# Kernel tuning notes

Measured on AMD Instinct MI355X. Metric: run time of the kernel, lower is better.

Reference implementation:

```python
import jax, jax.numpy as jnp
import numpy as np

C = 1024        # BIGNET_DIM
GS = 128        # group_size
R = 4           # lora_dim
NL = 12         # 4 blocks x 3 QLoRALinear
N = 4096        # batch
NG = C * C // GS  # 8192 groups per layer
EPS = 1e-5


def dequant4(q4, norm):
    # q4: [NG, GS//2] int32 in [0,255] (two nibbles per byte), norm: [NG,1] f32
    low = q4 & 0xF
    high = (q4 >> 4) & 0xF
    # interleave: even positions = low nibble, odd = high nibble
    q8 = jnp.stack([low, high], axis=-1).reshape(q4.shape[0], GS)
    w = (q8.astype(jnp.float32) / 15.0 * 2.0 - 1.0) * norm
    return w.reshape(C, C)  # [out_features, in_features]


def qlora_linear(x, q4, norm, a, b):
    # base 4-bit dequant matmul + low-rank LoRA add (bias=False)
    w = dequant4(q4, norm)
    return x @ w.T + (x @ a.T) @ b.T  # [N,C]


def block(x, q4s, norms, As, Bs):
    h = qlora_linear(x, q4s[0], norms[0], As[0], Bs[0])
    h = jax.nn.relu(h)
    h = qlora_linear(h, q4s[1], norms[1], As[1], Bs[1])
    h = jax.nn.relu(h)
    h = qlora_linear(h, q4s[2], norms[2], As[2], Bs[2])
    return h + x  # residual


def layer_norm(x, g, b):
    mu = jnp.mean(x, axis=-1, keepdims=True)
    var = jnp.var(x, axis=-1, keepdims=True)
    return (x - mu) * jax.lax.rsqrt(var + EPS) * g + b


def setup_inputs() -> dict:
    key = jax.random.key(0)
    ks = jax.random.split(key, 5)
    x = jax.random.normal(ks[0], (N, C), dtype=jnp.float32)
    w_q4 = jax.random.randint(ks[1], (NL, NG, GS // 2), 0, 256, dtype=jnp.int32)
    w_norm = jax.random.uniform(ks[2], (NL, NG, 1), dtype=jnp.float32, minval=0.01, maxval=0.1)
    lora_a = jax.random.normal(ks[3], (NL, R, C), dtype=jnp.float32) * 0.02
    lora_b = jax.random.normal(ks[4], (NL, C, R), dtype=jnp.float32) * 0.02
    ln_g = jnp.ones((2, C), dtype=jnp.float32)
    ln_b = jnp.zeros((2, C), dtype=jnp.float32)
    return {"x": x, "w_q4": w_q4, "w_norm": w_norm, "lora_a": lora_a,
            "lora_b": lora_b, "ln_g": ln_g, "ln_b": ln_b}


def reference(x, w_q4, w_norm, lora_a, lora_b, ln_g, ln_b):
    h = block(x, w_q4[0:3], w_norm[0:3], lora_a[0:3], lora_b[0:3])
    h = layer_norm(h, ln_g[0], ln_b[0])
    h = block(h, w_q4[3:6], w_norm[3:6], lora_a[3:6], lora_b[3:6])
    h = block(h, w_q4[6:9], w_norm[6:9], lora_a[6:9], lora_b[6:9])
    h = layer_norm(h, ln_g[1], ln_b[1])
    h = block(h, w_q4[9:12], w_norm[9:12], lora_a[9:12], lora_b[9:12])
    return h
```

## Files before the change

### kernel.cpp

```cpp
#include <hip/hip_runtime.h>

#define CD 1024
#define NB 4096

typedef __attribute__((ext_vector_type(8))) short short8;
typedef __attribute__((ext_vector_type(4))) short short4v;
typedef __attribute__((ext_vector_type(4))) float f32x4;
typedef __attribute__((ext_vector_type(4))) int int4v;

typedef __attribute__((address_space(1))) const void gv_t;
typedef __attribute__((address_space(3))) void lv_t;
#define GLOAD16(g, l) __builtin_amdgcn_global_load_lds((gv_t*)(g), (lv_t*)(l), 16, 0, 0)

__device__ __forceinline__ short f2bf(float f) {
  unsigned u = __float_as_uint(f);
  u = (u + 0x7FFFu + ((u >> 16) & 1u)) >> 16;
  return (short)u;
}
__device__ __forceinline__ float bf2f(short s) {
  return __uint_as_float(((unsigned)(unsigned short)s) << 16);
}

__global__ __launch_bounds__(256) void cvtx_kernel(const float* __restrict__ x,
                                                   short* __restrict__ xb) {
  int i = (blockIdx.x * 256 + threadIdx.x) * 8;
  f32x4 a = *(const f32x4*)(x + i);
  f32x4 b = *(const f32x4*)(x + i + 4);
  short8 o;
  o[0] = f2bf(a[0]); o[1] = f2bf(a[1]); o[2] = f2bf(a[2]); o[3] = f2bf(a[3]);
  o[4] = f2bf(b[0]); o[5] = f2bf(b[1]); o[6] = f2bf(b[2]); o[7] = f2bf(b[3]);
  *(short8*)(xb + i) = o;
}

__global__ __launch_bounds__(256) void deq_kernel(const int* __restrict__ q4,
                                                  const float* __restrict__ nrm,
                                                  const float* __restrict__ la,
                                                  const float* __restrict__ lb,
                                                  short* __restrict__ Wb) {
  int tidg = blockIdx.x * 256 + threadIdx.x;
  int w0 = tidg * 4;
  int l = w0 >> 19;
  int wl = w0 & 524287;
  int g = wl >> 6;
  int j0 = wl & 63;
  int o = g >> 3;
  int kb = ((g & 7) << 7) + (j0 << 1);
  int4v q = *(const int4v*)(q4 + w0);
  float n = nrm[(l << 13) + g];
  float s = n * (2.0f / 15.0f);
  f32x4 B = *(const f32x4*)(lb + (((l << 10) + o) << 2));
  const float* A = la + (l << 12);
  float Ar[4][8];
#pragma unroll
  for (int r = 0; r < 4; ++r) {
    f32x4 u = *(const f32x4*)(A + r * CD + kb);
    f32x4 v = *(const f32x4*)(A + r * CD + kb + 4);
    Ar[r][0] = u[0]; Ar[r][1] = u[1]; Ar[r][2] = u[2]; Ar[r][3] = u[3];
    Ar[r][4] = v[0]; Ar[r][5] = v[1]; Ar[r][6] = v[2]; Ar[r][7] = v[3];
  }
  short8 outv;
#pragma unroll
  for (int p = 0; p < 8; ++p) {
    int qw = q[p >> 1];
    int nib = (qw >> ((p & 1) << 2)) & 15;
    float wv = (float)nib * s - n;
    wv += B[0] * Ar[0][p] + B[1] * Ar[1][p] + B[2] * Ar[2][p] + B[3] * Ar[3][p];
    outv[p] = f2bf(wv);
  }
  *(short8*)(Wb + (l << 20) + (o << 10) + kb) = outv;
}

template <int EPI>
__global__ __launch_bounds__(256) void qgemm(const short* __restrict__ Act,
                                             const short* __restrict__ W,
                                             const short* __restrict__ Res,
                                             void* __restrict__ Out) {
  __shared__ __align__(16) short lds[2][2][128 * 64];
  const int tid = threadIdx.x;
  const int lane = tid & 63;
  const int wid = tid >> 6;
  const int wr = wid >> 1, wc = wid & 1;
  const int m0 = blockIdx.x * 128;
  const int o0 = blockIdx.y * 128;

  const int srow = (wid << 5) + (lane >> 3);
  const int gch = (lane & 7) ^ (lane >> 3);
  const short* aptr[4];
  const short* bptr[4];
#pragma unroll
  for (int i = 0; i < 4; ++i) {
    int r = srow + i * 8;
    aptr[i] = Act + (long)(m0 + r) * CD + (gch << 3);
    bptr[i] = W + (long)(o0 + r) * CD + (gch << 3);
  }

  auto stage = [&](int t, int buf) {
    const int koff = t << 6;
#pragma unroll
    for (int i = 0; i < 4; ++i) {
      GLOAD16(aptr[i] + koff, &lds[buf][0][((wid << 5) + (i << 3)) << 6]);
      GLOAD16(bptr[i] + koff, &lds[buf][1][((wid << 5) + (i << 3)) << 6]);
    }
  };

  f32x4 acc[4][4] = {};
  const int frow = lane & 15;
  const int fch = lane >> 4;
  const int fsw = lane & 7;

  stage(0, 0);
  for (int t = 0; t < 16; ++t) {
    __syncthreads();
    if (t < 15) stage(t + 1, (t + 1) & 1);
    const short* La = lds[t & 1][0];
    const short* Lb = lds[t & 1][1];
#pragma unroll
    for (int kk = 0; kk < 2; ++kk) {
      short8 af[4], bfr[4];
#pragma unroll
      for (int m = 0; m < 4; ++m) {
        int row = (wr << 6) + (m << 4) + frow;
        int ch = ((kk << 2) + fch) ^ fsw;
        af[m] = *(const short8*)(La + (row << 6) + (ch << 3));
      }
#pragma unroll
      for (int nn = 0; nn < 4; ++nn) {
        int row = (wc << 6) + (nn << 4) + frow;
        int ch = ((kk << 2) + fch) ^ fsw;
        bfr[nn] = *(const short8*)(Lb + (row << 6) + (ch << 3));
      }
#pragma unroll
      for (int m = 0; m < 4; ++m)
#pragma unroll
        for (int nn = 0; nn < 4; ++nn)
          acc[m][nn] = __builtin_amdgcn_mfma_f32_16x16x32_bf16(af[m], bfr[nn], acc[m][nn], 0, 0, 0);
    }
  }

  const int colb = o0 + (wc << 6) + frow;
  const int rowb = m0 + (wr << 6) + (fch << 2);
#pragma unroll
  for (int m = 0; m < 4; ++m) {
#pragma unroll
    for (int nn = 0; nn < 4; ++nn) {
#pragma unroll
      for (int r = 0; r < 4; ++r) {
        int row = rowb + (m << 4) + r;
        int col = colb + (nn << 4);
        float v = acc[m][nn][r];
        if (EPI == 0) {
          v = fmaxf(v, 0.0f);
          ((short*)Out)[(long)row * CD + col] = f2bf(v);
        } else if (EPI == 2) {
          v += bf2f(Res[(long)row * CD + col]);
          ((short*)Out)[(long)row * CD + col] = f2bf(v);
        } else {
          v += bf2f(Res[(long)row * CD + col]);
          ((float*)Out)[(long)row * CD + col] = v;
        }
      }
    }
  }
}

__global__ __launch_bounds__(256) void ln_kernel(const short* __restrict__ in,
                                                 short* __restrict__ out,
                                                 const float* __restrict__ g,
                                                 const float* __restrict__ b) {
  __shared__ float rs_[4], rq_[4];
  int row = blockIdx.x, tid = threadIdx.x;
  int k = tid * 4;
  short4v v = *(const short4v*)(in + (long)row * CD + k);
  float f0 = bf2f(v[0]), f1 = bf2f(v[1]), f2 = bf2f(v[2]), f3 = bf2f(v[3]);
  float s = f0 + f1 + f2 + f3;
  float q = f0 * f0 + f1 * f1 + f2 * f2 + f3 * f3;
#pragma unroll
  for (int off = 1; off < 64; off <<= 1) {
    s += __shfl_xor(s, off);
    q += __shfl_xor(q, off);
  }
  if ((tid & 63) == 0) { rs_[tid >> 6] = s; rq_[tid >> 6] = q; }
  __syncthreads();
  s = rs_[0] + rs_[1] + rs_[2] + rs_[3];
  q = rq_[0] + rq_[1] + rq_[2] + rq_[3];
  float mu = s * (1.0f / 1024.0f);
  float var = q * (1.0f / 1024.0f) - mu * mu;
  float rstd = rsqrtf(var + 1e-5f);
  short4v o;
  o[0] = f2bf((f0 - mu) * rstd * g[k] + b[k]);
  o[1] = f2bf((f1 - mu) * rstd * g[k + 1] + b[k + 1]);
  o[2] = f2bf((f2 - mu) * rstd * g[k + 2] + b[k + 2]);
  o[3] = f2bf((f3 - mu) * rstd * g[k + 3] + b[k + 3]);
  *(short4v*)(out + (long)row * CD + k) = o;
}

extern "C" void kernel_launch(void* const* d_in, const int* in_sizes, int n_in,
                              void* d_out, int out_size, void* d_ws, size_t ws_size,
                              hipStream_t stream) {
  const float* x = (const float*)d_in[0];
  const int* q4 = (const int*)d_in[1];
  const float* nrm = (const float*)d_in[2];
  const float* la = (const float*)d_in[3];
  const float* lb = (const float*)d_in[4];
  const float* lng = (const float*)d_in[5];
  const float* lnb = (const float*)d_in[6];

  short* Wb = (short*)d_ws;
  short* buf0 = (short*)((char*)d_ws + (24u << 20));
  short* buf1 = buf0 + (long)NB * CD;
  short* buf2 = (short*)d_out;
  short* buf3 = buf2 + (long)NB * CD;
  float* outf = (float*)d_out;

  cvtx_kernel<<<dim3(2048), dim3(256), 0, stream>>>(x, buf0);
  deq_kernel<<<dim3(6144), dim3(256), 0, stream>>>(q4, nrm, la, lb, Wb);

  dim3 gg(32, 8), bb(256);
  auto Wl = [&](int l) { return Wb + ((long)l << 20); };

  qgemm<0><<<gg, bb, 0, stream>>>(buf0, Wl(0), nullptr, buf1);
  qgemm<0><<<gg, bb, 0, stream>>>(buf1, Wl(1), nullptr, buf2);
  qgemm<2><<<gg, bb, 0, stream>>>(buf2, Wl(2), buf0, buf3);
  ln_kernel<<<dim3(4096), dim3(256), 0, stream>>>(buf3, buf0, lng, lnb);
  qgemm<0><<<gg, bb, 0, stream>>>(buf0, Wl(3), nullptr, buf1);
  qgemm<0><<<gg, bb, 0, stream>>>(buf1, Wl(4), nullptr, buf2);
  qgemm<2><<<gg, bb, 0, stream>>>(buf2, Wl(5), buf0, buf3);
  qgemm<0><<<gg, bb, 0, stream>>>(buf3, Wl(6), nullptr, buf1);
  qgemm<0><<<gg, bb, 0, stream>>>(buf1, Wl(7), nullptr, buf2);
  qgemm<2><<<gg, bb, 0, stream>>>(buf2, Wl(8), buf3, buf0);
  ln_kernel<<<dim3(4096), dim3(256), 0, stream>>>(buf0, buf1, lng + CD, lnb + CD);
  qgemm<0><<<gg, bb, 0, stream>>>(buf1, Wl(9), nullptr, buf2);
  qgemm<0><<<gg, bb, 0, stream>>>(buf2, Wl(10), nullptr, buf0);
  qgemm<3><<<gg, bb, 0, stream>>>(buf0, Wl(11), buf1, (void*)outf);
}
```

Before: 297.7 us.

## Shrink GEMM tile to 128x64, swap MFMA operands for vector epilogue, merge prep kernels

```diff
diff --git a/kernel.cpp b/kernel.cpp
--- a/kernel.cpp
+++ b/kernel.cpp
@@ -21,23 +21,25 @@
   return __uint_as_float(((unsigned)(unsigned short)s) << 16);
 }
 
-__global__ __launch_bounds__(256) void cvtx_kernel(const float* __restrict__ x,
-                                                   short* __restrict__ xb) {
-  int i = (blockIdx.x * 256 + threadIdx.x) * 8;
-  f32x4 a = *(const f32x4*)(x + i);
-  f32x4 b = *(const f32x4*)(x + i + 4);
-  short8 o;
-  o[0] = f2bf(a[0]); o[1] = f2bf(a[1]); o[2] = f2bf(a[2]); o[3] = f2bf(a[3]);
-  o[4] = f2bf(b[0]); o[5] = f2bf(b[1]); o[6] = f2bf(b[2]); o[7] = f2bf(b[3]);
-  *(short8*)(xb + i) = o;
-}
-
-__global__ __launch_bounds__(256) void deq_kernel(const int* __restrict__ q4,
-                                                  const float* __restrict__ nrm,
-                                                  const float* __restrict__ la,
-                                                  const float* __restrict__ lb,
-                                                  short* __restrict__ Wb) {
-  int tidg = blockIdx.x * 256 + threadIdx.x;
+__global__ __launch_bounds__(256) void prep_kernel(const float* __restrict__ x,
+                                                   short* __restrict__ xb,
+                                                   const int* __restrict__ q4,
+                                                   const float* __restrict__ nrm,
+                                                   const float* __restrict__ la,
+                                                   const float* __restrict__ lb,
+                                                   short* __restrict__ Wb) {
+  int bid = blockIdx.x;
+  if (bid < 2048) {
+    int i = (bid * 256 + threadIdx.x) * 8;
+    f32x4 a = *(const f32x4*)(x + i);
+    f32x4 b = *(const f32x4*)(x + i + 4);
+    short8 o;
+    o[0] = f2bf(a[0]); o[1] = f2bf(a[1]); o[2] = f2bf(a[2]); o[3] = f2bf(a[3]);
+    o[4] = f2bf(b[0]); o[5] = f2bf(b[1]); o[6] = f2bf(b[2]); o[7] = f2bf(b[3]);
+    *(short8*)(xb + i) = o;
+    return;
+  }
+  int tidg = (bid - 2048) * 256 + threadIdx.x;
   int w0 = tidg * 4;
   int l = w0 >> 19;
   int wl = w0 & 524287;
@@ -71,39 +73,35 @@
 }
 
 template <int EPI>
-__global__ __launch_bounds__(256) void qgemm(const short* __restrict__ Act,
-                                             const short* __restrict__ W,
-                                             const short* __restrict__ Res,
-                                             void* __restrict__ Out) {
-  __shared__ __align__(16) short lds[2][2][128 * 64];
+__global__ __launch_bounds__(256, 2) void qgemm(const short* __restrict__ Act,
+                                                const short* __restrict__ W,
+                                                const short* __restrict__ Res,
+                                                void* __restrict__ Out) {
+  __shared__ __align__(16) short ldsA[2][128 * 64];
+  __shared__ __align__(16) short ldsB[2][64 * 64];
   const int tid = threadIdx.x;
   const int lane = tid & 63;
   const int wid = tid >> 6;
   const int wr = wid >> 1, wc = wid & 1;
   const int m0 = blockIdx.x * 128;
-  const int o0 = blockIdx.y * 128;
-
-  const int srow = (wid << 5) + (lane >> 3);
-  const int gch = (lane & 7) ^ (lane >> 3);
-  const short* aptr[4];
-  const short* bptr[4];
-#pragma unroll
-  for (int i = 0; i < 4; ++i) {
-    int r = srow + i * 8;
-    aptr[i] = Act + (long)(m0 + r) * CD + (gch << 3);
-    bptr[i] = W + (long)(o0 + r) * CD + (gch << 3);
-  }
+  const int o0 = blockIdx.y * 64;
+
+  const int srow = tid >> 3;
+  const int gch = (tid & 7) ^ (srow & 7);
+  const short* abase = Act + (long)(m0 + srow) * CD + (gch << 3);
+  const short* bbase = W + (long)(o0 + srow) * CD + (gch << 3);
 
   auto stage = [&](int t, int buf) {
     const int koff = t << 6;
 #pragma unroll
-    for (int i = 0; i < 4; ++i) {
-      GLOAD16(aptr[i] + koff, &lds[buf][0][((wid << 5) + (i << 3)) << 6]);
-      GLOAD16(bptr[i] + koff, &lds[buf][1][((wid << 5) + (i << 3)) << 6]);
-    }
+    for (int i = 0; i < 4; ++i)
+      GLOAD16(abase + ((long)(i << 5)) * CD + koff, &ldsA[buf][(tid + (i << 8)) << 3]);
+#pragma unroll
+    for (int i = 0; i < 2; ++i)
+      GLOAD16(bbase + ((long)(i << 5)) * CD + koff, &ldsB[buf][(tid + (i << 8)) << 3]);
   };
 
-  f32x4 acc[4][4] = {};
+  f32x4 acc[4][2] = {};
   const int frow = lane & 15;
   const int fch = lane >> 4;
   const int fsw = lane & 7;
@@ -112,52 +110,62 @@
   for (int t = 0; t < 16; ++t) {
     __syncthreads();
     if (t < 15) stage(t + 1, (t + 1) & 1);
-    const short* La = lds[t & 1][0];
-    const short* Lb = lds[t & 1][1];
+    const short* La = ldsA[t & 1];
+    const short* Lb = ldsB[t & 1];
 #pragma unroll
     for (int kk = 0; kk < 2; ++kk) {
-      short8 af[4], bfr[4];
+      const int chb = (kk << 2) + fch;
+      short8 af[4], wf[2];
 #pragma unroll
       for (int m = 0; m < 4; ++m) {
         int row = (wr << 6) + (m << 4) + frow;
-        int ch = ((kk << 2) + fch) ^ fsw;
-        af[m] = *(const short8*)(La + (row << 6) + (ch << 3));
+        af[m] = *(const short8*)(La + (row << 6) + ((chb ^ fsw) << 3));
       }
 #pragma unroll
-      for (int nn = 0; nn < 4; ++nn) {
-        int row = (wc << 6) + (nn << 4) + frow;
-        int ch = ((kk << 2) + fch) ^ fsw;
-        bfr[nn] = *(const short8*)(Lb + (row << 6) + (ch << 3));
+      for (int n = 0; n < 2; ++n) {
+        int row = (wc << 5) + (n << 4) + frow;
+        wf[n] = *(const short8*)(Lb + (row << 6) + ((chb ^ fsw) << 3));
       }
 #pragma unroll
       for (int m = 0; m < 4; ++m)
 #pragma unroll
-        for (int nn = 0; nn < 4; ++nn)
-          acc[m][nn] = __builtin_amdgcn_mfma_f32_16x16x32_bf16(af[m], bfr[nn], acc[m][nn], 0, 0, 0);
+        for (int n = 0; n < 2; ++n)
+          acc[m][n] = __builtin_amdgcn_mfma_f32_16x16x32_bf16(wf[n], af[m], acc[m][n], 0, 0, 0);
     }
   }
 
-  const int colb = o0 + (wc << 6) + frow;
-  const int rowb = m0 + (wr << 6) + (fch << 2);
+  const int orow = m0 + (wr << 6) + frow;
+  const int ocol = o0 + (wc << 5) + (fch << 2);
 #pragma unroll
   for (int m = 0; m < 4; ++m) {
 #pragma unroll
-    for (int nn = 0; nn < 4; ++nn) {
-#pragma unroll
-      for (int r = 0; r < 4; ++r) {
-        int row = rowb + (m << 4) + r;
-        int col = colb + (nn << 4);
-        float v = acc[m][nn][r];
-        if (EPI == 0) {
-          v = fmaxf(v, 0.0f);
-          ((short*)Out)[(long)row * CD + col] = f2bf(v);
-        } else if (EPI == 2) {
-          v += bf2f(Res[(long)row * CD + col]);
-          ((short*)Out)[(long)row * CD + col] = f2bf(v);
-        } else {
-          v += bf2f(Res[(long)row * CD + col]);
-          ((float*)Out)[(long)row * CD + col] = v;
-        }
+    for (int n = 0; n < 2; ++n) {
+      long row = orow + (m << 4);
+      int col = ocol + (n << 4);
+      f32x4 v = acc[m][n];
+      if (EPI == 0) {
+        short4v ov;
+        ov[0] = f2bf(fmaxf(v[0], 0.0f));
+        ov[1] = f2bf(fmaxf(v[1], 0.0f));
+        ov[2] = f2bf(fmaxf(v[2], 0.0f));
+        ov[3] = f2bf(fmaxf(v[3], 0.0f));
+        *(short4v*)((short*)Out + row * CD + col) = ov;
+      } else if (EPI == 2) {
+        short4v rv = *(const short4v*)(Res + row * CD + col);
+        short4v ov;
+        ov[0] = f2bf(v[0] + bf2f(rv[0]));
+        ov[1] = f2bf(v[1] + bf2f(rv[1]));
+        ov[2] = f2bf(v[2] + bf2f(rv[2]));
+        ov[3] = f2bf(v[3] + bf2f(rv[3]));
+        *(short4v*)((short*)Out + row * CD + col) = ov;
+      } else {
+        short4v rv = *(const short4v*)(Res + row * CD + col);
+        f32x4 ov;
+        ov[0] = v[0] + bf2f(rv[0]);
+        ov[1] = v[1] + bf2f(rv[1]);
+        ov[2] = v[2] + bf2f(rv[2]);
+        ov[3] = v[3] + bf2f(rv[3]);
+        *(f32x4*)((float*)Out + row * CD + col) = ov;
       }
     }
   }
@@ -212,10 +220,9 @@
   short* buf3 = buf2 + (long)NB * CD;
   float* outf = (float*)d_out;
 
-  cvtx_kernel<<<dim3(2048), dim3(256), 0, stream>>>(x, buf0);
-  deq_kernel<<<dim3(6144), dim3(256), 0, stream>>>(q4, nrm, la, lb, Wb);
-
-  dim3 gg(32, 8), bb(256);
+  prep_kernel<<<dim3(8192), dim3(256), 0, stream>>>(x, buf0, q4, nrm, la, lb, Wb);
+
+  dim3 gg(32, 16), bb(256);
   auto Wl = [&](int l) { return Wb + ((long)l << 20); };
 
   qgemm<0><<<gg, bb, 0, stream>>>(buf0, Wl(0), nullptr, buf1);
```

New measurement: 322.4 us. 1.08x slower.
